# Kernel optimization log

Hardware: AMD Instinct MI355X
Metric: run time of the kernel (lower is better)

## Reference

```python
import jax, jax.numpy as jnp
import numpy as np

C, N, B = 16, 65536, 4096  # cases, points per case, batch of case IDs


def _w(key, fan_in, fan_out):
    return jax.random.normal(key, (fan_in, fan_out), dtype=jnp.float32) / np.sqrt(fan_in).astype(np.float32)


def setup_inputs() -> dict:
    key = jax.random.key(0)
    ks = jax.random.split(key, 8)
    pts = jax.random.normal(ks[0], (C, N, 3), dtype=jnp.float32)
    inp = {
        "pts": pts,
        "W1_0": _w(ks[1], 3, 64), "b1_0": jnp.zeros((64,), jnp.float32),
        "W1_1": _w(ks[2], 64, 128), "b1_1": jnp.zeros((128,), jnp.float32),
        "W1_2": _w(ks[3], 128, 512), "b1_2": jnp.zeros((512,), jnp.float32),
        "W2_0": _w(ks[4], 512, 256), "b2_0": jnp.zeros((256,), jnp.float32),
        "W2_1": _w(ks[5], 256, 512), "b2_1": jnp.zeros((512,), jnp.float32),
        "x": jax.random.randint(ks[6], (B,), 0, C, dtype=jnp.int64),
    }
    return inp


def reference(pts, W1_0, b1_0, W1_1, b1_1, W1_2, b1_2, W2_0, b2_0, W2_1, b2_1, x):
    def mlp1(h):  # shared per-point MLP, SiLU after every layer
        h = jax.nn.silu(h @ W1_0 + b1_0)
        h = jax.nn.silu(h @ W1_1 + b1_1)
        h = jax.nn.silu(h @ W1_2 + b1_2)
        return h

    feats = mlp1(pts)                       # [C, N, F1]
    idx = jnp.argmax(feats, axis=1)         # [C, F1] critical-point indices per feature
    # gather critical points (detached in the torch original)
    fixed = jax.lax.stop_gradient(pts[jnp.arange(pts.shape[0])[:, None], idx])  # [C, F1, 3]

    feats2 = mlp1(fixed)                    # [C, F1, F1]
    latent0 = jnp.max(feats2, axis=1)       # [C, F1]

    h = jax.nn.silu(latent0 @ W2_0 + b2_0)  # [C, 256]
    latent = h @ W2_1 + b2_1                # [C, total_modes*ge_features]

    caseID_unit = jax.nn.one_hot(x, latent.shape[0], dtype=latent.dtype)  # [B, C]
    return caseID_unit @ latent             # [B, 512]
```

## Files before the change

### kernel.cpp

```cpp
#include <hip/hip_runtime.h>
#include <math.h>

#define NCASES   16
#define NPTS_BIG 65536
#define F1       512
#define OUT_B    4096

typedef __attribute__((ext_vector_type(8))) short  short8;
typedef __attribute__((ext_vector_type(4))) float  floatx4;

__device__ __forceinline__ float silu_f(float x) {
    return x * __builtin_amdgcn_rcpf(1.0f + __expf(-x));
}

__device__ __forceinline__ unsigned f2bf_hi(float x) {
    unsigned u = __float_as_uint(x);
    return u + 0x7FFFu + ((u >> 16) & 1u);
}
__device__ __forceinline__ unsigned short f2bf(float x) {
    return (unsigned short)(f2bf_hi(x) >> 16);
}
__device__ __forceinline__ unsigned pk2bf_rtz(float lo, float hi) {
    return __builtin_amdgcn_perm(__float_as_uint(hi), __float_as_uint(lo), 0x07060302u);
}

__device__ __forceinline__ unsigned enc_f(float x) {
    unsigned u = __float_as_uint(x);
    return (u & 0x80000000u) ? ~u : (u | 0x80000000u);
}
__device__ __forceinline__ float dec_f(unsigned e) {
    unsigned u = (e & 0x80000000u) ? (e ^ 0x80000000u) : ~e;
    return __uint_as_float(u);
}

__device__ __forceinline__ float sgpr_f(float x) {
    return __uint_as_float(__builtin_amdgcn_readfirstlane(__float_as_uint(x)));
}

__global__ void k_prep(const float* __restrict__ W11, const float* __restrict__ W12,
                       unsigned short* __restrict__ BbWs, unsigned short* __restrict__ BcWs,
                       unsigned long long* __restrict__ argBufs)
{
    int i = blockIdx.x * 256 + threadIdx.x;
    if (i < 16384) argBufs[i] = 0ull;
    {
        int j = i & 7, l = (i >> 3) & 63, t = i >> 9;
        int KT = t & 3, NT = (t >> 2) & 3, w = t >> 4;
        int k = KT * 32 + (l >> 4) * 8 + j;
        int f = w * 64 + NT * 16 + (l & 15);
        BcWs[i] = f2bf(W12[(size_t)k * 512 + f]);
    }
    if (i < 8192) {
        int j = i & 7, l = (i >> 3) & 63, t = i >> 9;
        int KT = t & 1, w = t >> 1;
        int k = KT * 32 + (l >> 4) * 8 + j;
        int f = w * 16 + (l & 15);
        BbWs[i] = f2bf(W11[(size_t)k * 128 + f]);
    }
}

template<bool GATHER>
__global__ __launch_bounds__(512, 4)
void k_mlp1_argmax(const float* __restrict__ pts, int nPts, int chunksPerBlock,
                   const unsigned long long* __restrict__ gatherIdx,
                   const float* __restrict__ W10, const float* __restrict__ b10,
                   const float* __restrict__ b11, const float* __restrict__ b12,
                   const unsigned short* __restrict__ BbWs,
                   const unsigned short* __restrict__ BcWs,
                   unsigned long long* __restrict__ argOut)
{
    const int c   = blockIdx.y;
    const int tid = threadIdx.x;
    const int w   = tid >> 6;
    const int l   = tid & 63;
    const int lm  = l & 15;
    const int q   = l >> 4;

    __shared__ __align__(16) unsigned short s_h0[64][72];
    __shared__ __align__(16) unsigned short s_h1[64][136];

    const int wf = __builtin_amdgcn_readfirstlane(w);

    float wA0[8], wA1[8], wA2[8], bA[8];
    #pragma unroll
    for (int j = 0; j < 8; ++j) {
        wA0[j] = sgpr_f(W10[  0 + wf * 8 + j]);
        wA1[j] = sgpr_f(W10[ 64 + wf * 8 + j]);
        wA2[j] = sgpr_f(W10[128 + wf * 8 + j]);
        bA[j]  = sgpr_f(b10[       wf * 8 + j]);
    }

    short8 Bc[16];
    #pragma unroll
    for (int t = 0; t < 16; ++t)
        Bc[t] = *(const short8*)(BcWs + (size_t)((wf * 16 + t) * 64 + l) * 8);
    short8 Bb[2];
    #pragma unroll
    for (int t = 0; t < 2; ++t)
        Bb[t] = *(const short8*)(BbWs + (size_t)((wf * 2 + t) * 64 + l) * 8);

    const float bias11 = b11[wf * 16 + lm];

    float bestv[4];
    #pragma unroll
    for (int NT = 0; NT < 4; ++NT) bestv[NT] = -INFINITY;

    const float* cpts = pts + (size_t)c * nPts * 3;

    for (int ch = 0; ch < chunksPerBlock; ++ch) {
        const int pbase = (blockIdx.x * chunksPerBlock + ch) * 64;

        {
            float x, y, z;
            if (GATHER) {
                unsigned gi = ~(unsigned)(gatherIdx[(size_t)c * 512 + pbase + l] & 0xFFFFFFFFull);
                const float* sp = cpts + (size_t)gi * 3;
                x = sp[0]; y = sp[1]; z = sp[2];
            } else {
                const float* sp = cpts + (size_t)(pbase + l) * 3;
                x = sp[0]; y = sp[1]; z = sp[2];
            }
            float v[8];
            #pragma unroll
            for (int j = 0; j < 8; ++j) {
                float t = fmaf(z, wA2[j], bA[j]);
                t = fmaf(y, wA1[j], t);
                t = fmaf(x, wA0[j], t);
                v[j] = silu_f(t);
            }
            uint4 hv = { pk2bf_rtz(v[0], v[1]), pk2bf_rtz(v[2], v[3]),
                         pk2bf_rtz(v[4], v[5]), pk2bf_rtz(v[6], v[7]) };
            *(uint4*)&s_h0[l][wf * 8] = hv;
        }
        __syncthreads();

        #pragma unroll
        for (int MT = 0; MT < 4; ++MT) {
            short8 a0 = *(const short8*)&s_h0[MT * 16 + lm][q * 8];
            short8 a1 = *(const short8*)&s_h0[MT * 16 + lm][32 + q * 8];
            floatx4 acc = {bias11, bias11, bias11, bias11};
            acc = __builtin_amdgcn_mfma_f32_16x16x32_bf16(a0, Bb[0], acc, 0, 0, 0);
            acc = __builtin_amdgcn_mfma_f32_16x16x32_bf16(a1, Bb[1], acc, 0, 0, 0);
            #pragma unroll
            for (int r = 0; r < 4; ++r) {
                unsigned uv = __float_as_uint(silu_f(acc[r]));
                s_h1[MT * 16 + q * 4 + r][wf * 16 + lm] = (unsigned short)(uv >> 16);
            }
        }
        __syncthreads();

        const int cb0 = 127 - (ch << 4);
        #pragma unroll
        for (int MT = 0; MT < 4; ++MT) {
            short8 a[4];
            #pragma unroll
            for (int KT = 0; KT < 4; ++KT)
                a[KT] = *(const short8*)&s_h1[MT * 16 + lm][KT * 32 + q * 8];
            const int cbM = cb0 - (MT << 2);
            #pragma unroll
            for (int NT = 0; NT < 4; ++NT) {
                floatx4 acc = {0.f, 0.f, 0.f, 0.f};
                #pragma unroll
                for (int KT = 0; KT < 4; ++KT)
                    acc = __builtin_amdgcn_mfma_f32_16x16x32_bf16(a[KT], Bc[NT * 4 + KT], acc, 0, 0, 0);
                float x0 = __uint_as_float((__float_as_uint(acc[0]) & 0xFFFFFF80u) | (unsigned)(cbM));
                float x1 = __uint_as_float((__float_as_uint(acc[1]) & 0xFFFFFF80u) | (unsigned)(cbM - 1));
                float x2 = __uint_as_float((__float_as_uint(acc[2]) & 0xFFFFFF80u) | (unsigned)(cbM - 2));
                float x3 = __uint_as_float((__float_as_uint(acc[3]) & 0xFFFFFF80u) | (unsigned)(cbM - 3));
                float t0 = fmaxf(fmaxf(x0, x1), x2);
                bestv[NT] = fmaxf(fmaxf(t0, x3), bestv[NT]);
            }
        }
    }

    #pragma unroll
    for (int NT = 0; NT < 4; ++NT) {
        unsigned u = __float_as_uint(bestv[NT]);
        int t = 127 - (int)(u & 127u);
        unsigned idx = (unsigned)((blockIdx.x * chunksPerBlock + (t >> 4)) * 64
                                  + ((t >> 2) & 3) * 16 + q * 4 + (t & 3));
        float v = __uint_as_float(u & 0xFFFFFF80u) + b12[wf * 64 + NT * 16 + lm];
        #pragma unroll
        for (int m = 16; m <= 32; m <<= 1) {
            float    vo = __shfl_xor(v, m, 64);
            unsigned io = __shfl_xor(idx, m, 64);
            if (vo > v || (vo == v && io < idx)) { v = vo; idx = io; }
        }
        if (q == 0) {
            unsigned long long key = ((unsigned long long)enc_f(v) << 32)
                                   | (unsigned long long)(~idx);
            atomicMax(&argOut[(size_t)c * 512 + wf * 64 + NT * 16 + lm], key);
        }
    }
}

__global__ __launch_bounds__(256)
void k_head(const unsigned long long* __restrict__ argBuf2,
            const float* __restrict__ W20, const float* __restrict__ b20,
            const float* __restrict__ W21, const float* __restrict__ b21,
            float* __restrict__ latent)
{
    const int c = blockIdx.x, tid = threadIdx.x;
    __shared__ float l0[512];
    __shared__ float hh[256];
    l0[tid]       = silu_f(dec_f((unsigned)(argBuf2[(size_t)c * 512 + tid] >> 32)));
    l0[tid + 256] = silu_f(dec_f((unsigned)(argBuf2[(size_t)c * 512 + tid + 256] >> 32)));
    __syncthreads();
    float acc = b20[tid];
    for (int k = 0; k < 512; ++k) acc += l0[k] * W20[(size_t)k * 256 + tid];
    hh[tid] = silu_f(acc);
    __syncthreads();
    #pragma unroll
    for (int r = 0; r < 2; ++r) {
        int f = tid + r * 256;
        float a2 = b21[f];
        for (int k = 0; k < 256; ++k) a2 += hh[k] * W21[(size_t)k * 512 + f];
        latent[(size_t)c * 512 + f] = a2;
    }
}

__global__ void k_scatter(const int* __restrict__ x,
                          const float* __restrict__ latent,
                          float* __restrict__ out)
{
    const int b = blockIdx.x, t = threadIdx.x;
    int cid = x[b];
    const float4* src = (const float4*)(latent + (size_t)cid * 512);
    float4* dst = (float4*)(out + (size_t)b * 512);
    dst[t] = src[t];
}

extern "C" void kernel_launch(void* const* d_in, const int* in_sizes, int n_in,
                              void* d_out, int out_size, void* d_ws, size_t ws_size,
                              hipStream_t stream)
{
    const float* pts = (const float*)d_in[0];
    const float* W10 = (const float*)d_in[1];
    const float* b10 = (const float*)d_in[2];
    const float* W11 = (const float*)d_in[3];
    const float* b11 = (const float*)d_in[4];
    const float* W12 = (const float*)d_in[5];
    const float* b12 = (const float*)d_in[6];
    const float* W20 = (const float*)d_in[7];
    const float* b20 = (const float*)d_in[8];
    const float* W21 = (const float*)d_in[9];
    const float* b21 = (const float*)d_in[10];
    const int*   x   = (const int*)d_in[11];
    float* out = (float*)d_out;

    char* ws = (char*)d_ws;
    unsigned long long* argBuf  = (unsigned long long*)ws;
    unsigned long long* argBuf2 = (unsigned long long*)(ws + 65536);
    float* latent               = (float*)(ws + 131072);
    unsigned short* BbWs        = (unsigned short*)(ws + 163840);
    unsigned short* BcWs        = (unsigned short*)(ws + 180224);

    k_prep<<<dim3(256), dim3(256), 0, stream>>>(W11, W12, BbWs, BcWs, argBuf);

    k_mlp1_argmax<false><<<dim3(128, NCASES), dim3(512), 0, stream>>>(
        pts, NPTS_BIG, 8, nullptr, W10, b10, b11, b12, BbWs, BcWs, argBuf);

    k_mlp1_argmax<true><<<dim3(8, NCASES), dim3(512), 0, stream>>>(
        pts, NPTS_BIG, 1, argBuf, W10, b10, b11, b12, BbWs, BcWs, argBuf2);

    k_head<<<dim3(NCASES), dim3(256), 0, stream>>>(argBuf2, W20, b20, W21, b21, latent);

    k_scatter<<<dim3(OUT_B), dim3(128), 0, stream>>>(x, latent, out);
}
```

Measured before the change: 268.9 us.

## Double-buffer shared-memory stages to halve barriers and prefetch next chunk points

Shared-memory buffers for the first two MLP layers are doubled so that the next chunk's point load and first-layer compute happen during the current chunk's second layer. This removes one __syncthreads per chunk and hides global load latency behind MFMA work. The cost is double the LDS footprint, which may limit occupancy at 4 blocks of 512 threads, plus extra registers for the prefetched coordinates.

```diff
diff --git a/kernel.cpp b/kernel.cpp
--- a/kernel.cpp
+++ b/kernel.cpp
@@ -76,8 +76,8 @@
     const int lm  = l & 15;
     const int q   = l >> 4;
 
-    __shared__ __align__(16) unsigned short s_h0[64][72];
-    __shared__ __align__(16) unsigned short s_h1[64][136];
+    __shared__ __align__(16) unsigned short s_h0[2][64][72];
+    __shared__ __align__(16) unsigned short s_h1[2][64][136];
 
     const int wf = __builtin_amdgcn_readfirstlane(w);
 
@@ -100,6 +100,8 @@
         Bb[t] = *(const short8*)(BbWs + (size_t)((wf * 2 + t) * 64 + l) * 8);
 
     const float bias11 = b11[wf * 16 + lm];
+    const floatx4 bias4 = {bias11, bias11, bias11, bias11};
+    const floatx4 zero4 = {0.f, 0.f, 0.f, 0.f};
 
     float bestv[4];
     #pragma unroll
@@ -107,46 +109,60 @@
 
     const float* cpts = pts + (size_t)c * nPts * 3;
 
+    auto ldpt = [&](int ch, float& x, float& y, float& z) {
+        const int pbase = (blockIdx.x * chunksPerBlock + ch) * 64;
+        if (GATHER) {
+            unsigned gi = ~(unsigned)(gatherIdx[(size_t)c * 512 + pbase + l] & 0xFFFFFFFFull);
+            const float* sp = cpts + (size_t)gi * 3;
+            x = sp[0]; y = sp[1]; z = sp[2];
+        } else {
+            const float* sp = cpts + (size_t)(pbase + l) * 3;
+            x = sp[0]; y = sp[1]; z = sp[2];
+        }
+    };
+    auto stageA = [&](int p, float x, float y, float z) {
+        float v[8];
+        #pragma unroll
+        for (int j = 0; j < 8; ++j) {
+            float t = fmaf(z, wA2[j], bA[j]);
+            t = fmaf(y, wA1[j], t);
+            t = fmaf(x, wA0[j], t);
+            v[j] = silu_f(t);
+        }
+        uint4 hv = { pk2bf_rtz(v[0], v[1]), pk2bf_rtz(v[2], v[3]),
+                     pk2bf_rtz(v[4], v[5]), pk2bf_rtz(v[6], v[7]) };
+        *(uint4*)&s_h0[p][l][wf * 8] = hv;
+    };
+
+    {
+        float x, y, z;
+        ldpt(0, x, y, z);
+        stageA(0, x, y, z);
+    }
+    __syncthreads();
+
     for (int ch = 0; ch < chunksPerBlock; ++ch) {
-        const int pbase = (blockIdx.x * chunksPerBlock + ch) * 64;
-
-        {
-            float x, y, z;
-            if (GATHER) {
-                unsigned gi = ~(unsigned)(gatherIdx[(size_t)c * 512 + pbase + l] & 0xFFFFFFFFull);
-                const float* sp = cpts + (size_t)gi * 3;
-                x = sp[0]; y = sp[1]; z = sp[2];
-            } else {
-                const float* sp = cpts + (size_t)(pbase + l) * 3;
-                x = sp[0]; y = sp[1]; z = sp[2];
-            }
-            float v[8];
-            #pragma unroll
-            for (int j = 0; j < 8; ++j) {
-                float t = fmaf(z, wA2[j], bA[j]);
-                t = fmaf(y, wA1[j], t);
-                t = fmaf(x, wA0[j], t);
-                v[j] = silu_f(t);
-            }
-            uint4 hv = { pk2bf_rtz(v[0], v[1]), pk2bf_rtz(v[2], v[3]),
-                         pk2bf_rtz(v[4], v[5]), pk2bf_rtz(v[6], v[7]) };
-            *(uint4*)&s_h0[l][wf * 8] = hv;
-        }
-        __syncthreads();
+        const int p = ch & 1;
+        const bool more = (ch + 1 < chunksPerBlock);
+
+        float nx, ny, nz;
+        if (more) ldpt(ch + 1, nx, ny, nz);
 
         #pragma unroll
         for (int MT = 0; MT < 4; ++MT) {
-            short8 a0 = *(const short8*)&s_h0[MT * 16 + lm][q * 8];
-            short8 a1 = *(const short8*)&s_h0[MT * 16 + lm][32 + q * 8];
-            floatx4 acc = {bias11, bias11, bias11, bias11};
-            acc = __builtin_amdgcn_mfma_f32_16x16x32_bf16(a0, Bb[0], acc, 0, 0, 0);
+            short8 a0 = *(const short8*)&s_h0[p][MT * 16 + lm][q * 8];
+            short8 a1 = *(const short8*)&s_h0[p][MT * 16 + lm][32 + q * 8];
+            floatx4 acc = __builtin_amdgcn_mfma_f32_16x16x32_bf16(a0, Bb[0], bias4, 0, 0, 0);
             acc = __builtin_amdgcn_mfma_f32_16x16x32_bf16(a1, Bb[1], acc, 0, 0, 0);
             #pragma unroll
             for (int r = 0; r < 4; ++r) {
                 unsigned uv = __float_as_uint(silu_f(acc[r]));
-                s_h1[MT * 16 + q * 4 + r][wf * 16 + lm] = (unsigned short)(uv >> 16);
+                s_h1[p][MT * 16 + q * 4 + r][wf * 16 + lm] = (unsigned short)(uv >> 16);
             }
         }
+
+        if (more) stageA(p ^ 1, nx, ny, nz);
+
         __syncthreads();
 
         const int cb0 = 127 - (ch << 4);
@@ -155,13 +171,13 @@
             short8 a[4];
             #pragma unroll
             for (int KT = 0; KT < 4; ++KT)
-                a[KT] = *(const short8*)&s_h1[MT * 16 + lm][KT * 32 + q * 8];
+                a[KT] = *(const short8*)&s_h1[p][MT * 16 + lm][KT * 32 + q * 8];
             const int cbM = cb0 - (MT << 2);
             #pragma unroll
             for (int NT = 0; NT < 4; ++NT) {
-                floatx4 acc = {0.f, 0.f, 0.f, 0.f};
+                floatx4 acc = __builtin_amdgcn_mfma_f32_16x16x32_bf16(a[0], Bc[NT * 4 + 0], zero4, 0, 0, 0);
                 #pragma unroll
-                for (int KT = 0; KT < 4; ++KT)
+                for (int KT = 1; KT < 4; ++KT)
                     acc = __builtin_amdgcn_mfma_f32_16x16x32_bf16(a[KT], Bc[NT * 4 + KT], acc, 0, 0, 0);
                 float x0 = __uint_as_float((__float_as_uint(acc[0]) & 0xFFFFFF80u) | (unsigned)(cbM));
                 float x1 = __uint_as_float((__float_as_uint(acc[1]) & 0xFFFFFF80u) | (unsigned)(cbM - 1));
```

After: 263.1 us. -2.2%, faster.

## Stream layer-3 weights in halves and double-buffer two chunks to raise occupancy

Applied to the files above, without the earlier changes.

Stops keeping all 16 layer-3 weight fragments and both layer-2 fragments in registers for the whole kernel. Each chunk-pair now reloads half of the layer-3 weights (8 fragments) from global memory per pass, and the layer-2 weights per stage. Two 64-point chunks are processed at once using double-buffered shared tiles, with the next points prefetched during the MFMA phase. The launch bound rises from 4 to 6 waves-per-SIMD. The aim is lower register pressure and higher occupancy, traded for repeated weight loads from cache and twice the shared memory.

```diff
diff --git a/kernel.cpp b/kernel.cpp
--- a/kernel.cpp
+++ b/kernel.cpp
@@ -8,6 +8,7 @@
 
 typedef __attribute__((ext_vector_type(8))) short  short8;
 typedef __attribute__((ext_vector_type(4))) float  floatx4;
+typedef unsigned short ush;
 
 __device__ __forceinline__ float silu_f(float x) {
     return x * __builtin_amdgcn_rcpf(1.0f + __expf(-x));
@@ -17,8 +18,8 @@
     unsigned u = __float_as_uint(x);
     return u + 0x7FFFu + ((u >> 16) & 1u);
 }
-__device__ __forceinline__ unsigned short f2bf(float x) {
-    return (unsigned short)(f2bf_hi(x) >> 16);
+__device__ __forceinline__ ush f2bf(float x) {
+    return (ush)(f2bf_hi(x) >> 16);
 }
 __device__ __forceinline__ unsigned pk2bf_rtz(float lo, float hi) {
     return __builtin_amdgcn_perm(__float_as_uint(hi), __float_as_uint(lo), 0x07060302u);
@@ -38,7 +39,7 @@
 }
 
 __global__ void k_prep(const float* __restrict__ W11, const float* __restrict__ W12,
-                       unsigned short* __restrict__ BbWs, unsigned short* __restrict__ BcWs,
+                       ush* __restrict__ BbWs, ush* __restrict__ BcWs,
                        unsigned long long* __restrict__ argBufs)
 {
     int i = blockIdx.x * 256 + threadIdx.x;
@@ -60,13 +61,13 @@
 }
 
 template<bool GATHER>
-__global__ __launch_bounds__(512, 4)
+__global__ __launch_bounds__(512, 6)
 void k_mlp1_argmax(const float* __restrict__ pts, int nPts, int chunksPerBlock,
                    const unsigned long long* __restrict__ gatherIdx,
                    const float* __restrict__ W10, const float* __restrict__ b10,
                    const float* __restrict__ b11, const float* __restrict__ b12,
-                   const unsigned short* __restrict__ BbWs,
-                   const unsigned short* __restrict__ BcWs,
+                   const ush* __restrict__ BbWs,
+                   const ush* __restrict__ BcWs,
                    unsigned long long* __restrict__ argOut)
 {
     const int c   = blockIdx.y;
@@ -76,8 +77,8 @@
     const int lm  = l & 15;
     const int q   = l >> 4;
 
-    __shared__ __align__(16) unsigned short s_h0[64][72];
-    __shared__ __align__(16) unsigned short s_h1[64][136];
+    __shared__ __align__(16) ush s_h0[2][64][72];
+    __shared__ __align__(16) ush s_h1[2][64][136];
 
     const int wf = __builtin_amdgcn_readfirstlane(w);
 
@@ -90,15 +91,6 @@
         bA[j]  = sgpr_f(b10[       wf * 8 + j]);
     }
 
-    short8 Bc[16];
-    #pragma unroll
-    for (int t = 0; t < 16; ++t)
-        Bc[t] = *(const short8*)(BcWs + (size_t)((wf * 16 + t) * 64 + l) * 8);
-    short8 Bb[2];
-    #pragma unroll
-    for (int t = 0; t < 2; ++t)
-        Bb[t] = *(const short8*)(BbWs + (size_t)((wf * 2 + t) * 64 + l) * 8);
-
     const float bias11 = b11[wf * 16 + lm];
 
     float bestv[4];
@@ -106,71 +98,121 @@
     for (int NT = 0; NT < 4; ++NT) bestv[NT] = -INFINITY;
 
     const float* cpts = pts + (size_t)c * nPts * 3;
-
-    for (int ch = 0; ch < chunksPerBlock; ++ch) {
+    const ush* BbG = BbWs + (size_t)((wf * 2) * 64 + l) * 8;
+    const ush* BcG = BcWs + (size_t)((wf * 16) * 64 + l) * 8;
+
+    auto ldpt = [&](int ch, float& x, float& y, float& z) {
         const int pbase = (blockIdx.x * chunksPerBlock + ch) * 64;
-
-        {
-            float x, y, z;
-            if (GATHER) {
-                unsigned gi = ~(unsigned)(gatherIdx[(size_t)c * 512 + pbase + l] & 0xFFFFFFFFull);
-                const float* sp = cpts + (size_t)gi * 3;
-                x = sp[0]; y = sp[1]; z = sp[2];
-            } else {
-                const float* sp = cpts + (size_t)(pbase + l) * 3;
-                x = sp[0]; y = sp[1]; z = sp[2];
-            }
-            float v[8];
-            #pragma unroll
-            for (int j = 0; j < 8; ++j) {
-                float t = fmaf(z, wA2[j], bA[j]);
-                t = fmaf(y, wA1[j], t);
-                t = fmaf(x, wA0[j], t);
-                v[j] = silu_f(t);
-            }
-            uint4 hv = { pk2bf_rtz(v[0], v[1]), pk2bf_rtz(v[2], v[3]),
-                         pk2bf_rtz(v[4], v[5]), pk2bf_rtz(v[6], v[7]) };
-            *(uint4*)&s_h0[l][wf * 8] = hv;
-        }
-        __syncthreads();
-
+        if (GATHER) {
+            unsigned gi = ~(unsigned)(gatherIdx[(size_t)c * 512 + pbase + l] & 0xFFFFFFFFull);
+            const float* sp = cpts + (size_t)gi * 3;
+            x = sp[0]; y = sp[1]; z = sp[2];
+        } else {
+            const float* sp = cpts + (size_t)(pbase + l) * 3;
+            x = sp[0]; y = sp[1]; z = sp[2];
+        }
+    };
+    auto stageA = [&](int p, float x, float y, float z) {
+        float v[8];
+        #pragma unroll
+        for (int j = 0; j < 8; ++j) {
+            float t = fmaf(z, wA2[j], bA[j]);
+            t = fmaf(y, wA1[j], t);
+            t = fmaf(x, wA0[j], t);
+            v[j] = silu_f(t);
+        }
+        uint4 hv = { pk2bf_rtz(v[0], v[1]), pk2bf_rtz(v[2], v[3]),
+                     pk2bf_rtz(v[4], v[5]), pk2bf_rtz(v[6], v[7]) };
+        *(uint4*)&s_h0[p][l][wf * 8] = hv;
+    };
+    auto stageB = [&](int p) {
+        short8 Bb0 = *(const short8*)(BbG);
+        short8 Bb1 = *(const short8*)(BbG + 512);
         #pragma unroll
         for (int MT = 0; MT < 4; ++MT) {
-            short8 a0 = *(const short8*)&s_h0[MT * 16 + lm][q * 8];
-            short8 a1 = *(const short8*)&s_h0[MT * 16 + lm][32 + q * 8];
+            short8 a0 = *(const short8*)&s_h0[p][MT * 16 + lm][q * 8];
+            short8 a1 = *(const short8*)&s_h0[p][MT * 16 + lm][32 + q * 8];
             floatx4 acc = {bias11, bias11, bias11, bias11};
-            acc = __builtin_amdgcn_mfma_f32_16x16x32_bf16(a0, Bb[0], acc, 0, 0, 0);
-            acc = __builtin_amdgcn_mfma_f32_16x16x32_bf16(a1, Bb[1], acc, 0, 0, 0);
+            acc = __builtin_amdgcn_mfma_f32_16x16x32_bf16(a0, Bb0, acc, 0, 0, 0);
+            acc = __builtin_amdgcn_mfma_f32_16x16x32_bf16(a1, Bb1, acc, 0, 0, 0);
             #pragma unroll
             for (int r = 0; r < 4; ++r) {
                 unsigned uv = __float_as_uint(silu_f(acc[r]));
-                s_h1[MT * 16 + q * 4 + r][wf * 16 + lm] = (unsigned short)(uv >> 16);
+                s_h1[p][MT * 16 + q * 4 + r][wf * 16 + lm] = (ush)(uv >> 16);
             }
         }
-        __syncthreads();
-
-        const int cb0 = 127 - (ch << 4);
-        #pragma unroll
-        for (int MT = 0; MT < 4; ++MT) {
-            short8 a[4];
+    };
+    auto cChunk = [&](const ush (*H1)[136], int cb0, const short8* Bg, float* bv, int MT) {
+        short8 a[4];
+        #pragma unroll
+        for (int KT = 0; KT < 4; ++KT)
+            a[KT] = *(const short8*)&H1[MT * 16 + lm][KT * 32 + q * 8];
+        const int cbM = cb0 - (MT << 2);
+        #pragma unroll
+        for (int NTl = 0; NTl < 2; ++NTl) {
+            floatx4 acc = {0.f, 0.f, 0.f, 0.f};
             #pragma unroll
             for (int KT = 0; KT < 4; ++KT)
-                a[KT] = *(const short8*)&s_h1[MT * 16 + lm][KT * 32 + q * 8];
-            const int cbM = cb0 - (MT << 2);
-            #pragma unroll
-            for (int NT = 0; NT < 4; ++NT) {
-                floatx4 acc = {0.f, 0.f, 0.f, 0.f};
-                #pragma unroll
-                for (int KT = 0; KT < 4; ++KT)
-                    acc = __builtin_amdgcn_mfma_f32_16x16x32_bf16(a[KT], Bc[NT * 4 + KT], acc, 0, 0, 0);
-                float x0 = __uint_as_float((__float_as_uint(acc[0]) & 0xFFFFFF80u) | (unsigned)(cbM));
-                float x1 = __uint_as_float((__float_as_uint(acc[1]) & 0xFFFFFF80u) | (unsigned)(cbM - 1));
-                float x2 = __uint_as_float((__float_as_uint(acc[2]) & 0xFFFFFF80u) | (unsigned)(cbM - 2));
-                float x3 = __uint_as_float((__float_as_uint(acc[3]) & 0xFFFFFF80u) | (unsigned)(cbM - 3));
-                float t0 = fmaxf(fmaxf(x0, x1), x2);
-                bestv[NT] = fmaxf(fmaxf(t0, x3), bestv[NT]);
-            }
-        }
+                acc = __builtin_amdgcn_mfma_f32_16x16x32_bf16(a[KT], Bg[NTl * 4 + KT], acc, 0, 0, 0);
+            float x0 = __uint_as_float((__float_as_uint(acc[0]) & 0xFFFFFF80u) | (unsigned)(cbM));
+            float x1 = __uint_as_float((__float_as_uint(acc[1]) & 0xFFFFFF80u) | (unsigned)(cbM - 1));
+            float x2 = __uint_as_float((__float_as_uint(acc[2]) & 0xFFFFFF80u) | (unsigned)(cbM - 2));
+            float x3 = __uint_as_float((__float_as_uint(acc[3]) & 0xFFFFFF80u) | (unsigned)(cbM - 3));
+            float t0 = fmaxf(fmaxf(x0, x1), x2);
+            bv[NTl] = fmaxf(fmaxf(t0, x3), bv[NTl]);
+        }
+    };
+    auto cHalf = [&](int chA, bool haveB, int halfIdx, float* bv) {
+        short8 Bg[8];
+        const ush* gb = BcG + (size_t)halfIdx * 8 * 512;
+        #pragma unroll
+        for (int t = 0; t < 8; ++t)
+            Bg[t] = *(const short8*)(gb + (size_t)t * 512);
+        const int cbA = 127 - (chA << 4);
+        const int cbB = 127 - ((chA + 1) << 4);
+        #pragma unroll 1
+        for (int MT = 0; MT < 4; ++MT) {
+            cChunk(s_h1[0], cbA, Bg, bv, MT);
+            if (haveB) cChunk(s_h1[1], cbB, Bg, bv, MT);
+        }
+    };
+
+    {
+        float x0, y0, z0, x1, y1, z1;
+        const bool h1c = (chunksPerBlock > 1);
+        ldpt(0, x0, y0, z0);
+        if (h1c) ldpt(1, x1, y1, z1);
+        stageA(0, x0, y0, z0);
+        if (h1c) stageA(1, x1, y1, z1);
+    }
+    __syncthreads();
+
+    const int P = chunksPerBlock >> 1;
+    for (int k = 0; k < P; ++k) {
+        const int c0 = 2 * k;
+        stageB(0);
+        __syncthreads();
+        stageB(1);
+        __syncthreads();
+        float ax, ay, az, bx, by, bz;
+        const bool hA = (c0 + 2 < chunksPerBlock);
+        const bool hB = (c0 + 3 < chunksPerBlock);
+        if (hA) ldpt(c0 + 2, ax, ay, az);
+        if (hB) ldpt(c0 + 3, bx, by, bz);
+        cHalf(c0, true, 0, &bestv[0]);
+        __builtin_amdgcn_sched_barrier(0);
+        cHalf(c0, true, 1, &bestv[2]);
+        if (hA) stageA(0, ax, ay, az);
+        if (hB) stageA(1, bx, by, bz);
+        __syncthreads();
+    }
+    if (chunksPerBlock & 1) {
+        const int c0 = chunksPerBlock - 1;
+        stageB(0);
+        __syncthreads();
+        cHalf(c0, false, 0, &bestv[0]);
+        __builtin_amdgcn_sched_barrier(0);
+        cHalf(c0, false, 1, &bestv[2]);
     }
 
     #pragma unroll
@@ -252,8 +294,8 @@
     unsigned long long* argBuf  = (unsigned long long*)ws;
     unsigned long long* argBuf2 = (unsigned long long*)(ws + 65536);
     float* latent               = (float*)(ws + 131072);
-    unsigned short* BbWs        = (unsigned short*)(ws + 163840);
-    unsigned short* BcWs        = (unsigned short*)(ws + 180224);
+    ush* BbWs                   = (ush*)(ws + 163840);
+    ush* BcWs                   = (ush*)(ws + 180224);
 
     k_prep<<<dim3(256), dim3(256), 0, stream>>>(W11, W12, BbWs, BcWs, argBuf);
 
```

Result: slower. 345.1 us (+28.3%).
